# Kernel tuning notes

Hardware: AMD Instinct MI355X
Metric: run time of the kernel (lower is better)

The kernel has to match this reference:

```python
import jax, jax.numpy as jnp
import numpy as np

B, T, C = 2, 2048, 1024
NH, NKV, HD = 16, 4, 64   # n_head, n_kv_head, head_dim
WIN_LEFT = 1024           # flash-attn window_size=(1024, 0), causal


def rmsnorm(x):
    # F.rms_norm with no weight: x / sqrt(mean(x^2) + eps), eps = dtype eps
    eps = jnp.finfo(x.dtype).eps
    return x * jax.lax.rsqrt(jnp.mean(x * x, axis=-1, keepdims=True) + eps)


def rope(x, cos, sin):
    # x: [B,T,H,D]; cos/sin: [T,1,D/2] broadcast over batch and heads
    d = x.shape[-1] // 2
    x1, x2 = x[..., :d], x[..., d:]
    return jnp.concatenate([x1 * cos + x2 * sin, -x1 * sin + x2 * cos], axis=-1)


def setup_inputs() -> dict:
    key = jax.random.key(0)
    ks = jax.random.split(key, 9)
    return {
        "x":  jax.random.normal(ks[0], (B, T, C), jnp.float32),
        "x0": jax.random.normal(ks[1], (B, T, C), jnp.float32),
        "ve": jax.random.normal(ks[2], (B, T, NKV, HD), jnp.float32),
        "cos": jax.random.normal(ks[3], (T, 1, HD // 2), jnp.float32),
        "sin": jax.random.normal(ks[4], (T, 1, HD // 2), jnp.float32),
        "Wq": jax.random.normal(ks[5], (NH * HD, C), jnp.float32) * 0.02,
        "Wk": jax.random.normal(ks[6], (NKV * HD, C), jnp.float32) * 0.02,
        "Wv": jax.random.normal(ks[7], (NKV * HD, C), jnp.float32) * 0.02,
        "Wo": jax.random.normal(ks[8], (C, C), jnp.float32) * 0.02,
    }


def reference(x, x0, ve, cos, sin, Wq, Wk, Wv, Wo):
    b, t, c = x.shape
    q = (x @ Wq.T).reshape(b, t, NH, HD)
    k = (x @ Wk.T).reshape(b, t, NKV, HD)
    v = (x @ Wv.T).reshape(b, t, NKV, HD)
    v_init = v
    # is_late branch: halve_value, add_init_qkv, add_init_v all active
    v = 0.5 * v
    x0n = rmsnorm(x0)
    q = 0.5 * q + 0.5 * (x0n @ Wq.T).reshape(b, t, NH, HD)
    k = 0.5 * k + 0.5 * (x0n @ Wk.T).reshape(b, t, NKV, HD)
    v = v + 0.5 * (x0n @ Wv.T).reshape(b, t, NKV, HD)
    v = v + 0.5 * ve
    # rotary -> rms-norm -> scale 1.2 on q and k
    q = rmsnorm(rope(q, cos, sin)) * 1.2
    k = rmsnorm(rope(k, cos, sin)) * 1.2
    # GQA: repeat kv heads to match query heads
    g = NH // NKV
    k = jnp.repeat(k, g, axis=2)
    v = jnp.repeat(v, g, axis=2)
    scores = jnp.einsum("bqhd,bkhd->bhqk", q, k) / np.float32(np.sqrt(HD))
    i = jnp.arange(t)[:, None]
    j = jnp.arange(t)[None, :]
    mask = (j <= i) & (i - j <= WIN_LEFT)  # causal sliding window
    scores = jnp.where(mask, scores, jnp.finfo(scores.dtype).min)
    att = jax.nn.softmax(scores, axis=-1)
    y = jnp.einsum("bhqk,bkhd->bqhd", att, v).reshape(b, t, c)
    y = y @ Wo.T
    return (y, v_init)
```

## Files before the change

kernel.cpp:

```cpp
#include <hip/hip_runtime.h>


typedef __attribute__((ext_vector_type(8))) short bf16x8;
typedef __attribute__((ext_vector_type(4))) float f32x4;
typedef unsigned short u16;
typedef unsigned int u32;

#define B_ 2
#define T_ 2048
#define C_ 1024
#define NH_ 16
#define NKV_ 4
#define WIN_ 1024
#define M_ (B_*T_)
#define EPS_ 1.1920929e-07f

__device__ __forceinline__ u16 f2bf(float f) {
  u32 u = __float_as_uint(f);
  u32 r = (u + 0x7fffu + ((u >> 16) & 1u)) >> 16;
  return (u16)r;
}
__device__ __forceinline__ float bf2f(u16 h) { return __uint_as_float(((u32)h) << 16); }

__device__ __forceinline__ void gload16(const u16* g, u16* l) {
  __builtin_amdgcn_global_load_lds((const __attribute__((address_space(1))) u32*)g,
                                   (__attribute__((address_space(3))) u32*)l, 16, 0, 0);
}
#define SWZ(row, kg) ((((row)) << 7) + ((((kg) ^ ((row) & 7))) << 4))
#define SWO(lane) (8 * (((lane) & 7) ^ (((lane) >> 3) & 7)))

__global__ __launch_bounds__(256) void k_convert_all(const float* __restrict__ Wq,
                                                     const float* __restrict__ Wk,
                                                     const float* __restrict__ Wv,
                                                     const float* __restrict__ Wo,
                                                     u16* __restrict__ dst) {
  int i4 = blockIdx.x * 256 + threadIdx.x;
  const float* src; int s0;
  if (i4 < 262144)      { src = Wq; s0 = 0; }
  else if (i4 < 327680) { src = Wk; s0 = 262144; }
  else if (i4 < 393216) { src = Wv; s0 = 327680; }
  else                  { src = Wo; s0 = 393216; }
  float4 v = ((const float4*)src)[i4 - s0];
  ushort4 o;
  o.x = f2bf(v.x); o.y = f2bf(v.y); o.z = f2bf(v.z); o.w = f2bf(v.w);
  ((ushort4*)dst)[i4] = o;
}

__global__ __launch_bounds__(256) void k_rms_combine(const float* __restrict__ x,
                                                     const float* __restrict__ x0,
                                                     u16* __restrict__ xbf,
                                                     u16* __restrict__ xmbf) {
  int row = blockIdx.x;
  int tid = threadIdx.x, lane = tid & 63, w = tid >> 6;
  const float4* px0 = (const float4*)(x0 + (size_t)row * C_);
  const float4* px  = (const float4*)(x  + (size_t)row * C_);
  float4 v0 = px0[tid];
  float ss = v0.x * v0.x + v0.y * v0.y + v0.z * v0.z + v0.w * v0.w;
  #pragma unroll
  for (int m = 1; m < 64; m <<= 1) ss += __shfl_xor(ss, m, 64);
  __shared__ float red[4];
  if (lane == 0) red[w] = ss;
  __syncthreads();
  float tot = red[0] + red[1] + red[2] + red[3];
  float rn = rsqrtf(tot * (1.0f / C_) + EPS_);
  float4 vx = px[tid];
  ushort4 om, ox;
  om.x = f2bf(0.5f * (vx.x + v0.x * rn));
  om.y = f2bf(0.5f * (vx.y + v0.y * rn));
  om.z = f2bf(0.5f * (vx.z + v0.z * rn));
  om.w = f2bf(0.5f * (vx.w + v0.w * rn));
  ox.x = f2bf(vx.x); ox.y = f2bf(vx.y); ox.z = f2bf(vx.z); ox.w = f2bf(vx.w);
  ((ushort4*)(xmbf + (size_t)row * C_))[tid] = om;
  ((ushort4*)(xbf  + (size_t)row * C_))[tid] = ox;
}

__device__ __forceinline__ void gemm_core(const u16* pa0, const u16* pb0,
                                          u16* Asl, u16* Bsl,
                                          int lane, int w, int r0, int c0,
                                          f32x4 acc[4][2]) {
  const char* Ab = (const char*)Asl;
  const char* Bb = (const char*)Bsl;
  for (int kt = 0; kt < 1024; kt += 64) {
    __syncthreads();
    #pragma unroll
    for (int c = 0; c < 4; c++)
      gload16(pa0 + (size_t)c * 32 * 1024 + kt, Asl + (c * 32 + w * 8) * 64);
    #pragma unroll
    for (int c = 0; c < 2; c++)
      gload16(pb0 + (size_t)c * 32 * 1024 + kt, Bsl + (c * 32 + w * 8) * 64);
    __syncthreads();
    bf16x8 af[2][4], bfr[2][2];
    #pragma unroll
    for (int ks = 0; ks < 2; ks++) {
      #pragma unroll
      for (int fi = 0; fi < 4; fi++)
        af[ks][fi] = *(const bf16x8*)(Ab + SWZ(r0 + fi * 16 + (lane & 15), ks * 4 + (lane >> 4)));
      #pragma unroll
      for (int fj = 0; fj < 2; fj++)
        bfr[ks][fj] = *(const bf16x8*)(Bb + SWZ(c0 + fj * 16 + (lane & 15), ks * 4 + (lane >> 4)));
    }
    #pragma unroll
    for (int ks = 0; ks < 2; ks++)
      #pragma unroll
      for (int fi = 0; fi < 4; fi++)
        #pragma unroll
        for (int fj = 0; fj < 2; fj++)
          acc[fi][fj] = __builtin_amdgcn_mfma_f32_16x16x32_bf16(af[ks][fi], bfr[ks][fj], acc[fi][fj], 0, 0, 0);
  }
}

__global__ __launch_bounds__(256) void k_gemm_qkv(const u16* __restrict__ xm,
                                                  const u16* __restrict__ xb,
                                                  const u16* __restrict__ Wq,
                                                  const u16* __restrict__ Wk,
                                                  const u16* __restrict__ Wv,
                                                  u16* __restrict__ qpre,
                                                  u16* __restrict__ kpre,
                                                  u16* __restrict__ vmid,
                                                  float* __restrict__ vinit) {
  __shared__ u16 Asl[128 * 64];
  __shared__ u16 Bsl[64 * 64];
  int tid = threadIdx.x, lane = tid & 63, w = tid >> 6;
  int m0 = blockIdx.x * 128, bn = blockIdx.y, n0 = bn * 64;
  const u16* A; const u16* Wseg; int nseg;
  if (bn < 16)      { A = xm; Wseg = Wq; nseg = n0; }
  else if (bn < 20) { A = xm; Wseg = Wk; nseg = n0 - 1024; }
  else if (bn < 24) { A = xm; Wseg = Wv; nseg = n0 - 1280; }
  else              { A = xb; Wseg = Wv; nseg = n0 - 1536; }
  int swo = SWO(lane);
  const u16* pa0 = A    + (size_t)(m0 + w * 8 + (lane >> 3)) * 1024 + swo;
  const u16* pb0 = Wseg + (size_t)(nseg + w * 8 + (lane >> 3)) * 1024 + swo;
  int r0 = (w >> 1) * 64, c0 = (w & 1) * 32;
  f32x4 acc[4][2] = {};
  gemm_core(pa0, pb0, Asl, Bsl, lane, w, r0, c0, acc);
  #pragma unroll
  for (int fi = 0; fi < 4; fi++)
    #pragma unroll
    for (int fj = 0; fj < 2; fj++)
      #pragma unroll
      for (int i = 0; i < 4; i++) {
        int m = m0 + r0 + fi * 16 + (lane >> 4) * 4 + i;
        int nl = nseg + c0 + fj * 16 + (lane & 15);
        float v = acc[fi][fj][i];
        if (bn < 16)      qpre[(size_t)m * 1024 + nl] = f2bf(v);
        else if (bn < 20) kpre[(size_t)m * 256 + nl] = f2bf(v);
        else if (bn < 24) vmid[(size_t)m * 256 + nl] = f2bf(v);
        else              vinit[(size_t)m * 256 + nl] = v;
      }
}

__global__ __launch_bounds__(256) void k_gemm_o(const u16* __restrict__ A,
                                                const u16* __restrict__ W,
                                                float* __restrict__ y) {
  __shared__ u16 Asl[128 * 64];
  __shared__ u16 Bsl[64 * 64];
  int tid = threadIdx.x, lane = tid & 63, w = tid >> 6;
  int m0 = blockIdx.x * 128, n0 = blockIdx.y * 64;
  int swo = SWO(lane);
  const u16* pa0 = A + (size_t)(m0 + w * 8 + (lane >> 3)) * 1024 + swo;
  const u16* pb0 = W + (size_t)(n0 + w * 8 + (lane >> 3)) * 1024 + swo;
  int r0 = (w >> 1) * 64, c0 = (w & 1) * 32;
  f32x4 acc[4][2] = {};
  gemm_core(pa0, pb0, Asl, Bsl, lane, w, r0, c0, acc);
  #pragma unroll
  for (int fi = 0; fi < 4; fi++)
    #pragma unroll
    for (int fj = 0; fj < 2; fj++)
      #pragma unroll
      for (int i = 0; i < 4; i++) {
        int m = m0 + r0 + fi * 16 + (lane >> 4) * 4 + i;
        int n = n0 + c0 + fj * 16 + (lane & 15);
        y[(size_t)m * 1024 + n] = acc[fi][fj][i];
      }
}

__global__ __launch_bounds__(256) void k_qk_post(const u16* __restrict__ qpre,
                                                 const u16* __restrict__ kpre,
                                                 const float* __restrict__ cosp,
                                                 const float* __restrict__ sinp,
                                                 u16* __restrict__ Qh,
                                                 u16* __restrict__ Kh) {
  int w = threadIdx.x >> 6, lane = threadIdx.x & 63;
  int vid = blockIdx.x * 4 + w;
  const int NQ = B_ * T_ * NH_;
  int t; float val; size_t dst; u16* out;
  if (vid < NQ) {
    int h = vid & 15; t = (vid >> 4) & 2047; int b = vid >> 15;
    val = bf2f(qpre[(size_t)vid * 64 + lane]);
    dst = (((size_t)(b * NH_ + h) * T_) + t) * 64 + lane;
    out = Qh;
  } else {
    int kid = vid - NQ;
    int hk = kid & 3; t = (kid >> 2) & 2047; int b = kid >> 13;
    val = bf2f(kpre[(size_t)kid * 64 + lane]);
    dst = (((size_t)(b * NKV_ + hk) * T_) + t) * 64 + lane;
    out = Kh;
  }
  int di = lane & 31;
  float partner = __shfl_xor(val, 32, 64);
  float c = cosp[t * 32 + di], s = sinp[t * 32 + di];
  float r = (lane < 32) ? (val * c + partner * s) : (val * c - partner * s);
  float ss = r * r;
  #pragma unroll
  for (int m2 = 1; m2 < 64; m2 <<= 1) ss += __shfl_xor(ss, m2, 64);
  r *= rsqrtf(ss * (1.0f / 64.0f) + EPS_) * 1.2f;
  out[dst] = f2bf(r);
}

__global__ __launch_bounds__(256) void k_vt(const u16* __restrict__ vmid,
                                            const float* __restrict__ ve,
                                            u16* __restrict__ VtG) {
  __shared__ u16 S[64][72];
  int tid = threadIdx.x;
  int t0 = blockIdx.x * 64, hk = blockIdx.y, b = blockIdx.z;
  {
    int tl = tid >> 2, dg = (tid & 3) * 16;
    const int4* pvm = (const int4*)(vmid + (size_t)(b * T_ + t0 + tl) * 256 + hk * 64 + dg);
    const float4* pve = (const float4*)(ve + ((size_t)(b * T_ + t0 + tl) * 4 + hk) * 64 + dg);
    int4 vv[2]; vv[0] = pvm[0]; vv[1] = pvm[1];
    const u16* vm = (const u16*)vv;
    float4 vf[4]; vf[0] = pve[0]; vf[1] = pve[1]; vf[2] = pve[2]; vf[3] = pve[3];
    const float* vfp = (const float*)vf;
    u16 r[16];
    #pragma unroll
    for (int e = 0; e < 16; e++) r[e] = f2bf(bf2f(vm[e]) + 0.5f * vfp[e]);
    *(int4*)&S[tl][dg] = *(int4*)&r[0];
    *(int4*)&S[tl][dg + 8] = *(int4*)&r[8];
  }
  __syncthreads();
  {
    int dl = tid >> 2, tg = (tid & 3) * 16;
    u16 r[16];
    #pragma unroll
    for (int j = 0; j < 16; j++) r[j] = S[tg + j][dl];
    u16* o = VtG + ((size_t)((b * NKV_ + hk) * 64 + dl)) * T_ + t0 + tg;
    *(int4*)&o[0] = *(int4*)&r[0];
    *(int4*)&o[8] = *(int4*)&r[8];
  }
}

__global__ __launch_bounds__(256) void k_attn(const u16* __restrict__ Qh,
                                              const u16* __restrict__ Kh,
                                              const u16* __restrict__ VtG,
                                              u16* __restrict__ ao) {
  __shared__ u16 Ksl[64 * 64];
  __shared__ u16 Vsl[64 * 64];
  __shared__ u16 Ps[4][16][72];
  int tid = threadIdx.x, lane = tid & 63, w = tid >> 6;
  int qt = (int)gridDim.x - 1 - (int)blockIdx.x;
  int h = blockIdx.y, b = blockIdx.z;
  int hk = h >> 2;
  int q0 = qt * 64;
  const u16* Qp = Qh + ((size_t)(b * NH_ + h) * T_) * 64;
  const u16* Kp = Kh + ((size_t)(b * NKV_ + hk) * T_) * 64;
  int swo = SWO(lane);
  const u16* pk0 = Kp + (size_t)(w * 8 + (lane >> 3)) * 64 + swo;
  const u16* pv0 = VtG + ((size_t)((b * NKV_ + hk) * 64 + w * 8 + (lane >> 3))) * T_ + swo;
  const char* Kb = (const char*)Ksl;
  const char* Vb = (const char*)Vsl;

  int qr = q0 + w * 16 + (lane & 15);
  bf16x8 qf[2];
  qf[0] = *(const bf16x8*)(Qp + (size_t)qr * 64 + (lane >> 4) * 8);
  qf[1] = *(const bf16x8*)(Qp + (size_t)qr * 64 + 32 + (lane >> 4) * 8);

  f32x4 o[4] = {};
  float mrun[4], lrun[4];
  #pragma unroll
  for (int i = 0; i < 4; i++) { mrun[i] = -1e4f; lrun[i] = 0.f; }
  int kt_lo = q0 - WIN_; if (kt_lo < 0) kt_lo = 0;

  for (int kt = kt_lo; kt <= q0; kt += 64) {
    __syncthreads();
    #pragma unroll
    for (int c = 0; c < 2; c++) {
      gload16(pk0 + (size_t)(kt + c * 32) * 64, Ksl + (c * 32 + w * 8) * 64);
      gload16(pv0 + kt + (size_t)c * 32 * T_,   Vsl + (c * 32 + w * 8) * 64);
    }
    __syncthreads();
    f32x4 s[4];
    #pragma unroll
    for (int ct = 0; ct < 4; ct++) {
      f32x4 z = {0.f, 0.f, 0.f, 0.f};
      s[ct] = z;
      #pragma unroll
      for (int ks = 0; ks < 2; ks++) {
        bf16x8 kf = *(const bf16x8*)(Kb + SWZ(ct * 16 + (lane & 15), ks * 4 + (lane >> 4)));
        s[ct] = __builtin_amdgcn_mfma_f32_16x16x32_bf16(qf[ks], kf, s[ct], 0, 0, 0);
      }
    }
    bool need_mask = (kt == q0) || (kt == q0 - WIN_);
    int irow0 = q0 + w * 16 + (lane >> 4) * 4;
    float tmax[4] = {-1e30f, -1e30f, -1e30f, -1e30f};
    if (need_mask) {
      #pragma unroll
      for (int ct = 0; ct < 4; ct++) {
        int j = kt + ct * 16 + (lane & 15);
        #pragma unroll
        for (int i = 0; i < 4; i++) {
          int irow = irow0 + i;
          bool valid = (j <= irow) && (irow - j <= WIN_);
          float sv = valid ? s[ct][i] * 0.125f : -1e9f;
          s[ct][i] = sv;
          tmax[i] = fmaxf(tmax[i], sv);
        }
      }
    } else {
      #pragma unroll
      for (int ct = 0; ct < 4; ct++)
        #pragma unroll
        for (int i = 0; i < 4; i++) {
          float sv = s[ct][i] * 0.125f;
          s[ct][i] = sv;
          tmax[i] = fmaxf(tmax[i], sv);
        }
    }
    #pragma unroll
    for (int i = 0; i < 4; i++) {
      #pragma unroll
      for (int m2 = 1; m2 < 16; m2 <<= 1) tmax[i] = fmaxf(tmax[i], __shfl_xor(tmax[i], m2, 64));
    }
    float alpha[4];
    #pragma unroll
    for (int i = 0; i < 4; i++) {
      float mn = fmaxf(mrun[i], tmax[i]);
      alpha[i] = __expf(mrun[i] - mn);
      mrun[i] = mn;
    }
    float rsum[4] = {0.f, 0.f, 0.f, 0.f};
    #pragma unroll
    for (int ct = 0; ct < 4; ct++)
      #pragma unroll
      for (int i = 0; i < 4; i++) {
        float p = __expf(s[ct][i] - mrun[i]);
        s[ct][i] = p;
        rsum[i] += p;
      }
    #pragma unroll
    for (int i = 0; i < 4; i++) {
      #pragma unroll
      for (int m2 = 1; m2 < 16; m2 <<= 1) rsum[i] += __shfl_xor(rsum[i], m2, 64);
      lrun[i] = lrun[i] * alpha[i] + rsum[i];
    }
    #pragma unroll
    for (int fj = 0; fj < 4; fj++)
      #pragma unroll
      for (int i = 0; i < 4; i++) o[fj][i] *= alpha[i];
    #pragma unroll
    for (int ct = 0; ct < 4; ct++)
      #pragma unroll
      for (int i = 0; i < 4; i++)
        Ps[w][(lane >> 4) * 4 + i][ct * 16 + (lane & 15)] = f2bf(s[ct][i]);
    bf16x8 pf[2];
    pf[0] = *(const bf16x8*)&Ps[w][lane & 15][(lane >> 4) * 8];
    pf[1] = *(const bf16x8*)&Ps[w][lane & 15][32 + (lane >> 4) * 8];
    #pragma unroll
    for (int fj = 0; fj < 4; fj++) {
      #pragma unroll
      for (int ks = 0; ks < 2; ks++) {
        bf16x8 vf = *(const bf16x8*)(Vb + SWZ(fj * 16 + (lane & 15), ks * 4 + (lane >> 4)));
        o[fj] = __builtin_amdgcn_mfma_f32_16x16x32_bf16(pf[ks], vf, o[fj], 0, 0, 0);
      }
    }
  }
  #pragma unroll
  for (int i = 0; i < 4; i++) {
    float inv = 1.0f / lrun[i];
    int irow = q0 + w * 16 + (lane >> 4) * 4 + i;
    size_t base = ((size_t)(b * T_ + irow) * NH_ + h) * 64;
    #pragma unroll
    for (int fj = 0; fj < 4; fj++)
      ao[base + fj * 16 + (lane & 15)] = f2bf(o[fj][i] * inv);
  }
}

extern "C" void kernel_launch(void* const* d_in, const int* in_sizes, int n_in,
                              void* d_out, int out_size, void* d_ws, size_t ws_size,
                              hipStream_t stream) {
  const float* x    = (const float*)d_in[0];
  const float* x0   = (const float*)d_in[1];
  const float* ve   = (const float*)d_in[2];
  const float* cosp = (const float*)d_in[3];
  const float* sinp = (const float*)d_in[4];
  const float* Wq   = (const float*)d_in[5];
  const float* Wk   = (const float*)d_in[6];
  const float* Wv   = (const float*)d_in[7];
  const float* Wo   = (const float*)d_in[8];
  float* out = (float*)d_out;

  u16* ws = (u16*)d_ws;
  size_t off = 0;
  u16* xbf  = ws + off; off += (size_t)M_ * C_;
  u16* xmbf = ws + off; off += (size_t)M_ * C_;
  u16* Wqb  = ws + off; off += (size_t)1024 * 1024;
  u16* Wkb  = ws + off; off += (size_t)256 * 1024;
  u16* Wvb  = ws + off; off += (size_t)256 * 1024;
  u16* Wob  = ws + off; off += (size_t)1024 * 1024;
  u16* qpre = ws + off; off += (size_t)M_ * 1024;
  u16* kpre = ws + off; off += (size_t)M_ * 256;
  u16* vmid = ws + off; off += (size_t)M_ * 256;
  u16* VtG  = ws + off; off += (size_t)B_ * NKV_ * 64 * T_;
  u16* aob = xbf;
  u16* Qhb = xmbf;
  u16* Khb = Wqb;

  k_convert_all<<<2560, 256, 0, stream>>>(Wq, Wk, Wv, Wo, Wqb);
  k_rms_combine<<<4096, 256, 0, stream>>>(x, x0, xbf, xmbf);
  k_gemm_qkv<<<dim3(32, 28), 256, 0, stream>>>(xmbf, xbf, Wqb, Wkb, Wvb,
                                               qpre, kpre, vmid, out + (size_t)M_ * C_);
  k_qk_post<<<20480, 256, 0, stream>>>(qpre, kpre, cosp, sinp, Qhb, Khb);
  k_vt<<<dim3(32, 4, 2), 256, 0, stream>>>(vmid, ve, VtG);
  k_attn<<<dim3(32, 16, 2), 256, 0, stream>>>(Qhb, Khb, VtG, aob);
  k_gemm_o<<<dim3(32, 16), 256, 0, stream>>>(aob, Wob, out);
}
```

Before: 218.7 us.

## Double-buffer GEMM and attention tiles, rewrite attention with 32x32 MFMA

Both GEMM kernels now double-buffer their shared-memory A/B tiles, prefetching the next K slice while computing the current one, which removes one barrier per iteration. The attention kernel is rewritten to use 512-thread blocks over 256 query rows, 32x32x16 MFMAs, transposed S=K·Q so probabilities stay in registers (shuffle-based repacking instead of an LDS round-trip), lazy rescaling of the running max, and double-buffered K/V tiles. The softmax scale 1/8 is folded into the Q post-processing scale (1.2*0.125). The change adds LDS use and register pressure and gives fewer, larger attention blocks, which may hurt load balance across the causal window.

```diff
diff --git a/kernel.cpp b/kernel.cpp
--- a/kernel.cpp
+++ b/kernel.cpp
@@ -3,6 +3,7 @@
 
 typedef __attribute__((ext_vector_type(8))) short bf16x8;
 typedef __attribute__((ext_vector_type(4))) float f32x4;
+typedef __attribute__((ext_vector_type(16))) float f32x16;
 typedef unsigned short u16;
 typedef unsigned int u32;
 
@@ -78,17 +79,24 @@
                                           u16* Asl, u16* Bsl,
                                           int lane, int w, int r0, int c0,
                                           f32x4 acc[4][2]) {
-  const char* Ab = (const char*)Asl;
-  const char* Bb = (const char*)Bsl;
+  #pragma unroll
+  for (int c = 0; c < 4; c++) gload16(pa0 + (size_t)c * 32 * 1024, Asl + (c * 32 + w * 8) * 64);
+  #pragma unroll
+  for (int c = 0; c < 2; c++) gload16(pb0 + (size_t)c * 32 * 1024, Bsl + (c * 32 + w * 8) * 64);
+  int cur = 0;
   for (int kt = 0; kt < 1024; kt += 64) {
     __syncthreads();
-    #pragma unroll
-    for (int c = 0; c < 4; c++)
-      gload16(pa0 + (size_t)c * 32 * 1024 + kt, Asl + (c * 32 + w * 8) * 64);
-    #pragma unroll
-    for (int c = 0; c < 2; c++)
-      gload16(pb0 + (size_t)c * 32 * 1024 + kt, Bsl + (c * 32 + w * 8) * 64);
-    __syncthreads();
+    if (kt + 64 < 1024) {
+      int nxt = cur ^ 1;
+      #pragma unroll
+      for (int c = 0; c < 4; c++)
+        gload16(pa0 + (size_t)c * 32 * 1024 + kt + 64, Asl + nxt * 8192 + (c * 32 + w * 8) * 64);
+      #pragma unroll
+      for (int c = 0; c < 2; c++)
+        gload16(pb0 + (size_t)c * 32 * 1024 + kt + 64, Bsl + nxt * 4096 + (c * 32 + w * 8) * 64);
+    }
+    const char* Ab = (const char*)(Asl + cur * 8192);
+    const char* Bb = (const char*)(Bsl + cur * 4096);
     bf16x8 af[2][4], bfr[2][2];
     #pragma unroll
     for (int ks = 0; ks < 2; ks++) {
@@ -106,6 +114,7 @@
         #pragma unroll
         for (int fj = 0; fj < 2; fj++)
           acc[fi][fj] = __builtin_amdgcn_mfma_f32_16x16x32_bf16(af[ks][fi], bfr[ks][fj], acc[fi][fj], 0, 0, 0);
+    cur ^= 1;
   }
 }
 
@@ -118,8 +127,8 @@
                                                   u16* __restrict__ kpre,
                                                   u16* __restrict__ vmid,
                                                   float* __restrict__ vinit) {
-  __shared__ u16 Asl[128 * 64];
-  __shared__ u16 Bsl[64 * 64];
+  __shared__ u16 Asl[2 * 8192];
+  __shared__ u16 Bsl[2 * 4096];
   int tid = threadIdx.x, lane = tid & 63, w = tid >> 6;
   int m0 = blockIdx.x * 128, bn = blockIdx.y, n0 = bn * 64;
   const u16* A; const u16* Wseg; int nseg;
@@ -152,8 +161,8 @@
 __global__ __launch_bounds__(256) void k_gemm_o(const u16* __restrict__ A,
                                                 const u16* __restrict__ W,
                                                 float* __restrict__ y) {
-  __shared__ u16 Asl[128 * 64];
-  __shared__ u16 Bsl[64 * 64];
+  __shared__ u16 Asl[2 * 8192];
+  __shared__ u16 Bsl[2 * 4096];
   int tid = threadIdx.x, lane = tid & 63, w = tid >> 6;
   int m0 = blockIdx.x * 128, n0 = blockIdx.y * 64;
   int swo = SWO(lane);
@@ -183,18 +192,18 @@
   int w = threadIdx.x >> 6, lane = threadIdx.x & 63;
   int vid = blockIdx.x * 4 + w;
   const int NQ = B_ * T_ * NH_;
-  int t; float val; size_t dst; u16* out;
+  int t; float val; size_t dst; u16* out; float scale;
   if (vid < NQ) {
     int h = vid & 15; t = (vid >> 4) & 2047; int b = vid >> 15;
     val = bf2f(qpre[(size_t)vid * 64 + lane]);
     dst = (((size_t)(b * NH_ + h) * T_) + t) * 64 + lane;
-    out = Qh;
+    out = Qh; scale = 0.15f;
   } else {
     int kid = vid - NQ;
     int hk = kid & 3; t = (kid >> 2) & 2047; int b = kid >> 13;
     val = bf2f(kpre[(size_t)kid * 64 + lane]);
     dst = (((size_t)(b * NKV_ + hk) * T_) + t) * 64 + lane;
-    out = Kh;
+    out = Kh; scale = 1.2f;
   }
   int di = lane & 31;
   float partner = __shfl_xor(val, 32, 64);
@@ -203,7 +212,7 @@
   float ss = r * r;
   #pragma unroll
   for (int m2 = 1; m2 < 64; m2 <<= 1) ss += __shfl_xor(ss, m2, 64);
-  r *= rsqrtf(ss * (1.0f / 64.0f) + EPS_) * 1.2f;
+  r *= rsqrtf(ss * (1.0f / 64.0f) + EPS_) * scale;
   out[dst] = f2bf(r);
 }
 
@@ -239,138 +248,126 @@
   }
 }
 
-__global__ __launch_bounds__(256) void k_attn(const u16* __restrict__ Qh,
+__global__ __launch_bounds__(512) void k_attn(const u16* __restrict__ Qh,
                                               const u16* __restrict__ Kh,
                                               const u16* __restrict__ VtG,
                                               u16* __restrict__ ao) {
-  __shared__ u16 Ksl[64 * 64];
-  __shared__ u16 Vsl[64 * 64];
-  __shared__ u16 Ps[4][16][72];
+  __shared__ u16 Ksl[2][64 * 64];
+  __shared__ u16 Vsl[2][64 * 64];
+  __shared__ float Sc[8][32];
   int tid = threadIdx.x, lane = tid & 63, w = tid >> 6;
-  int qt = (int)gridDim.x - 1 - (int)blockIdx.x;
-  int h = blockIdx.y, b = blockIdx.z;
+  int hi = lane >> 5, qc = lane & 31;
+  int qt = blockIdx.x, h = blockIdx.y, b = blockIdx.z;
   int hk = h >> 2;
-  int q0 = qt * 64;
+  int q0 = qt * 256, wq0 = q0 + w * 32;
   const u16* Qp = Qh + ((size_t)(b * NH_ + h) * T_) * 64;
   const u16* Kp = Kh + ((size_t)(b * NKV_ + hk) * T_) * 64;
   int swo = SWO(lane);
   const u16* pk0 = Kp + (size_t)(w * 8 + (lane >> 3)) * 64 + swo;
   const u16* pv0 = VtG + ((size_t)((b * NKV_ + hk) * 64 + w * 8 + (lane >> 3))) * T_ + swo;
-  const char* Kb = (const char*)Ksl;
-  const char* Vb = (const char*)Vsl;
-
-  int qr = q0 + w * 16 + (lane & 15);
-  bf16x8 qf[2];
-  qf[0] = *(const bf16x8*)(Qp + (size_t)qr * 64 + (lane >> 4) * 8);
-  qf[1] = *(const bf16x8*)(Qp + (size_t)qr * 64 + 32 + (lane >> 4) * 8);
-
-  f32x4 o[4] = {};
-  float mrun[4], lrun[4];
-  #pragma unroll
-  for (int i = 0; i < 4; i++) { mrun[i] = -1e4f; lrun[i] = 0.f; }
+
+  bf16x8 qf[4];
+  #pragma unroll
+  for (int ds = 0; ds < 4; ds++)
+    qf[ds] = *(const bf16x8*)(Qp + (size_t)(wq0 + qc) * 64 + ds * 16 + hi * 8);
+
+  f32x16 o0 = {}, o1 = {};
+  float mrun = -1e4f, lrun = 0.f;
   int kt_lo = q0 - WIN_; if (kt_lo < 0) kt_lo = 0;
-
-  for (int kt = kt_lo; kt <= q0; kt += 64) {
+  int kt_hi = q0 + 192;
+
+  gload16(pk0 + (size_t)kt_lo * 64, &Ksl[0][w * 512]);
+  gload16(pv0 + kt_lo,              &Vsl[0][w * 512]);
+  int cur = 0;
+  for (int kt = kt_lo; kt <= kt_hi; kt += 64) {
     __syncthreads();
-    #pragma unroll
-    for (int c = 0; c < 2; c++) {
-      gload16(pk0 + (size_t)(kt + c * 32) * 64, Ksl + (c * 32 + w * 8) * 64);
-      gload16(pv0 + kt + (size_t)c * 32 * T_,   Vsl + (c * 32 + w * 8) * 64);
+    if (kt + 64 <= kt_hi) {
+      gload16(pk0 + (size_t)(kt + 64) * 64, &Ksl[cur ^ 1][w * 512]);
+      gload16(pv0 + kt + 64,                &Vsl[cur ^ 1][w * 512]);
     }
-    __syncthreads();
-    f32x4 s[4];
-    #pragma unroll
-    for (int ct = 0; ct < 4; ct++) {
-      f32x4 z = {0.f, 0.f, 0.f, 0.f};
-      s[ct] = z;
-      #pragma unroll
-      for (int ks = 0; ks < 2; ks++) {
-        bf16x8 kf = *(const bf16x8*)(Kb + SWZ(ct * 16 + (lane & 15), ks * 4 + (lane >> 4)));
-        s[ct] = __builtin_amdgcn_mfma_f32_16x16x32_bf16(qf[ks], kf, s[ct], 0, 0, 0);
-      }
-    }
-    bool need_mask = (kt == q0) || (kt == q0 - WIN_);
-    int irow0 = q0 + w * 16 + (lane >> 4) * 4;
-    float tmax[4] = {-1e30f, -1e30f, -1e30f, -1e30f};
-    if (need_mask) {
-      #pragma unroll
-      for (int ct = 0; ct < 4; ct++) {
-        int j = kt + ct * 16 + (lane & 15);
-        #pragma unroll
-        for (int i = 0; i < 4; i++) {
-          int irow = irow0 + i;
-          bool valid = (j <= irow) && (irow - j <= WIN_);
-          float sv = valid ? s[ct][i] * 0.125f : -1e9f;
-          s[ct][i] = sv;
-          tmax[i] = fmaxf(tmax[i], sv);
+    if (kt <= wq0 + 31 && kt + 63 >= wq0 - WIN_) {
+      const char* Kb = (const char*)&Ksl[cur][0];
+      const char* Vb = (const char*)&Vsl[cur][0];
+      f32x16 st[2] = {};
+      #pragma unroll
+      for (int kt2 = 0; kt2 < 2; kt2++)
+        #pragma unroll
+        for (int ds = 0; ds < 4; ds++) {
+          bf16x8 kf = *(const bf16x8*)(Kb + SWZ(kt2 * 32 + qc, 2 * ds + hi));
+          st[kt2] = __builtin_amdgcn_mfma_f32_32x32x16_bf16(kf, qf[ds], st[kt2], 0, 0, 0);
+        }
+      bool full = (kt + 63 <= wq0) && (wq0 + 31 - kt <= WIN_);
+      int D0 = wq0 + qc - kt;
+      float p[2][16];
+      float tmax = -1e30f;
+      #pragma unroll
+      for (int kt2 = 0; kt2 < 2; kt2++)
+        #pragma unroll
+        for (int r = 0; r < 16; r++) {
+          float sv = st[kt2][r];
+          if (!full) {
+            int jl = 32 * kt2 + (r & 3) + 8 * (r >> 2) + 4 * hi;
+            sv = (jl <= D0 && jl >= D0 - WIN_) ? sv : -1e9f;
+          }
+          p[kt2][r] = sv;
+          tmax = fmaxf(tmax, sv);
+        }
+      tmax = fmaxf(tmax, __shfl_xor(tmax, 32, 64));
+      if (__any(tmax > mrun + 8.0f)) {
+        float mnew = fmaxf(mrun, tmax);
+        float alpha = __expf(mrun - mnew);
+        mrun = mnew; lrun *= alpha;
+        if (hi == 0) Sc[w][qc] = alpha;
+        #pragma unroll
+        for (int r = 0; r < 16; r++) {
+          float al = Sc[w][(r & 3) + 8 * (r >> 2) + 4 * hi];
+          o0[r] *= al; o1[r] *= al;
         }
       }
-    } else {
-      #pragma unroll
-      for (int ct = 0; ct < 4; ct++)
-        #pragma unroll
-        for (int i = 0; i < 4; i++) {
-          float sv = s[ct][i] * 0.125f;
-          s[ct][i] = sv;
-          tmax[i] = fmaxf(tmax[i], sv);
+      float rsum = 0.f;
+      u32 pw[2][8];
+      #pragma unroll
+      for (int kt2 = 0; kt2 < 2; kt2++)
+        #pragma unroll
+        for (int c = 0; c < 8; c++) {
+          float pe = __expf(p[kt2][2 * c] - mrun);
+          float po = __expf(p[kt2][2 * c + 1] - mrun);
+          rsum += pe + po;
+          pw[kt2][c] = __builtin_amdgcn_perm(__float_as_uint(po), __float_as_uint(pe), 0x07060302u);
+        }
+      rsum += __shfl_xor(rsum, 32, 64);
+      lrun += rsum;
+      #pragma unroll
+      for (int kt2 = 0; kt2 < 2; kt2++)
+        #pragma unroll
+        for (int ksp = 0; ksp < 2; ksp++) {
+          union { u32 uw[4]; bf16x8 v; } U;
+          #pragma unroll
+          for (int c = 0; c < 2; c++) {
+            u32 x = pw[kt2][4 * ksp + c];
+            u32 y = pw[kt2][4 * ksp + 2 + c];
+            u32 xs = (u32)__shfl_xor((int)x, 32, 64);
+            u32 ys = (u32)__shfl_xor((int)y, 32, 64);
+            U.uw[c]     = hi ? ys : x;
+            U.uw[2 + c] = hi ? y : xs;
+          }
+          int ks = 2 * kt2 + ksp;
+          bf16x8 v0 = *(const bf16x8*)(Vb + SWZ(qc,      2 * ks + hi));
+          bf16x8 v1 = *(const bf16x8*)(Vb + SWZ(32 + qc, 2 * ks + hi));
+          o0 = __builtin_amdgcn_mfma_f32_32x32x16_bf16(U.v, v0, o0, 0, 0, 0);
+          o1 = __builtin_amdgcn_mfma_f32_32x32x16_bf16(U.v, v1, o1, 0, 0, 0);
         }
     }
-    #pragma unroll
-    for (int i = 0; i < 4; i++) {
-      #pragma unroll
-      for (int m2 = 1; m2 < 16; m2 <<= 1) tmax[i] = fmaxf(tmax[i], __shfl_xor(tmax[i], m2, 64));
-    }
-    float alpha[4];
-    #pragma unroll
-    for (int i = 0; i < 4; i++) {
-      float mn = fmaxf(mrun[i], tmax[i]);
-      alpha[i] = __expf(mrun[i] - mn);
-      mrun[i] = mn;
-    }
-    float rsum[4] = {0.f, 0.f, 0.f, 0.f};
-    #pragma unroll
-    for (int ct = 0; ct < 4; ct++)
-      #pragma unroll
-      for (int i = 0; i < 4; i++) {
-        float p = __expf(s[ct][i] - mrun[i]);
-        s[ct][i] = p;
-        rsum[i] += p;
-      }
-    #pragma unroll
-    for (int i = 0; i < 4; i++) {
-      #pragma unroll
-      for (int m2 = 1; m2 < 16; m2 <<= 1) rsum[i] += __shfl_xor(rsum[i], m2, 64);
-      lrun[i] = lrun[i] * alpha[i] + rsum[i];
-    }
-    #pragma unroll
-    for (int fj = 0; fj < 4; fj++)
-      #pragma unroll
-      for (int i = 0; i < 4; i++) o[fj][i] *= alpha[i];
-    #pragma unroll
-    for (int ct = 0; ct < 4; ct++)
-      #pragma unroll
-      for (int i = 0; i < 4; i++)
-        Ps[w][(lane >> 4) * 4 + i][ct * 16 + (lane & 15)] = f2bf(s[ct][i]);
-    bf16x8 pf[2];
-    pf[0] = *(const bf16x8*)&Ps[w][lane & 15][(lane >> 4) * 8];
-    pf[1] = *(const bf16x8*)&Ps[w][lane & 15][32 + (lane >> 4) * 8];
-    #pragma unroll
-    for (int fj = 0; fj < 4; fj++) {
-      #pragma unroll
-      for (int ks = 0; ks < 2; ks++) {
-        bf16x8 vf = *(const bf16x8*)(Vb + SWZ(fj * 16 + (lane & 15), ks * 4 + (lane >> 4)));
-        o[fj] = __builtin_amdgcn_mfma_f32_16x16x32_bf16(pf[ks], vf, o[fj], 0, 0, 0);
-      }
-    }
-  }
-  #pragma unroll
-  for (int i = 0; i < 4; i++) {
-    float inv = 1.0f / lrun[i];
-    int irow = q0 + w * 16 + (lane >> 4) * 4 + i;
-    size_t base = ((size_t)(b * T_ + irow) * NH_ + h) * 64;
-    #pragma unroll
-    for (int fj = 0; fj < 4; fj++)
-      ao[base + fj * 16 + (lane & 15)] = f2bf(o[fj][i] * inv);
+    cur ^= 1;
+  }
+  if (hi == 0) Sc[w][qc] = 1.0f / lrun;
+  #pragma unroll
+  for (int r = 0; r < 16; r++) {
+    int q = (r & 3) + 8 * (r >> 2) + 4 * hi;
+    float il = Sc[w][q];
+    size_t base = ((size_t)(b * T_ + wq0 + q) * NH_ + h) * 64;
+    ao[base + qc]      = f2bf(o0[r] * il);
+    ao[base + 32 + qc] = f2bf(o1[r] * il);
   }
 }
 
@@ -410,6 +407,6 @@
                                                qpre, kpre, vmid, out + (size_t)M_ * C_);
   k_qk_post<<<20480, 256, 0, stream>>>(qpre, kpre, cosp, sinp, Qhb, Khb);
   k_vt<<<dim3(32, 4, 2), 256, 0, stream>>>(vmid, ve, VtG);
-  k_attn<<<dim3(32, 16, 2), 256, 0, stream>>>(Qhb, Khb, VtG, aob);
+  k_attn<<<dim3(8, 16, 2), 512, 0, stream>>>(Qhb, Khb, VtG, aob);
   k_gemm_o<<<dim3(32, 16), 256, 0, stream>>>(aob, Wob, out);
 }
```

Result: faster. 214.2 us (-2.1%).
